# Kernel tuning notes

Measured on AMD Instinct MI355X. Metric: run time of the kernel, lower is better.

## Reference

```python
import jax, jax.numpy as jnp
import numpy as np

E = 1024   # embed_dim
H = 16     # num_heads
DH = E // H
FF = 4096  # intermediate_size
EPS = 1e-5


def layernorm(x, g, b):
    mu = jnp.mean(x, axis=-1, keepdims=True)
    var = jnp.var(x, axis=-1, keepdims=True)
    return (x - mu) * jax.lax.rsqrt(var + EPS) * g + b


def setup_inputs() -> dict:
    key = jax.random.key(0)
    ks = jax.random.split(key, 16)
    s = 0.02
    return {
        "x": jax.random.normal(ks[0], (2, 2048, E), dtype=jnp.float32),
        "ln1_g": jnp.ones((E,), jnp.float32),
        "ln1_b": jnp.zeros((E,), jnp.float32),
        "ln2_g": jnp.ones((E,), jnp.float32),
        "ln2_b": jnp.zeros((E,), jnp.float32),
        # per-head Q/K/V projections stacked: [H, E, DH]
        "wq": jax.random.normal(ks[1], (H, E, DH), jnp.float32) * s,
        "bq": jnp.zeros((H, DH), jnp.float32),
        "wk": jax.random.normal(ks[2], (H, E, DH), jnp.float32) * s,
        "bk": jnp.zeros((H, DH), jnp.float32),
        "wv": jax.random.normal(ks[3], (H, E, DH), jnp.float32) * s,
        "bv": jnp.zeros((H, DH), jnp.float32),
        "wo": jax.random.normal(ks[4], (E, E), jnp.float32) * s,
        "bo": jnp.zeros((E,), jnp.float32),
        "w1": jax.random.normal(ks[5], (E, FF), jnp.float32) * s,
        "b1": jnp.zeros((FF,), jnp.float32),
        "w2": jax.random.normal(ks[6], (FF, E), jnp.float32) * s,
        "b2": jnp.zeros((E,), jnp.float32),
    }


def reference(x, ln1_g, ln1_b, ln2_g, ln2_b, wq, bq, wk, bk, wv, bv,
              wo, bo, w1, b1, w2, b2):
    # --- multi-head attention (pre-LN) ---
    h = layernorm(x, ln1_g, ln1_b)                       # [B,S,E]
    q = jnp.einsum('bse,hed->bhsd', h, wq) + bq[:, None, :]
    k = jnp.einsum('bse,hed->bhsd', h, wk) + bk[:, None, :]
    v = jnp.einsum('bse,hed->bhsd', h, wv) + bv[:, None, :]
    scores = jnp.einsum('bhsd,bhtd->bhst', q, k) / jnp.sqrt(
        jnp.asarray(DH, x.dtype))                        # [B,H,S,S]
    w = jax.nn.softmax(scores, axis=-1)
    attn = jnp.einsum('bhst,bhtd->bhsd', w, v)           # [B,H,S,DH]
    B, _, S, _ = attn.shape
    concat = attn.transpose(0, 2, 1, 3).reshape(B, S, E)  # head concat order
    x = x + concat @ wo + bo
    # --- feed-forward (pre-LN), exact GELU, dropout_p=0 ---
    h2 = layernorm(x, ln2_g, ln2_b)
    ff = jax.nn.gelu(h2 @ w1 + b1, approximate=False) @ w2 + b2
    return x + ff
```

## Files before the change

### kernel.cpp

```cpp
#include <hip/hip_runtime.h>
#include <hip/hip_bf16.h>
#include <math.h>

typedef __attribute__((ext_vector_type(8))) short short8;
typedef __attribute__((ext_vector_type(4))) float f32x4;
typedef __attribute__((ext_vector_type(16))) float f32x16;
typedef __attribute__((ext_vector_type(4))) unsigned u32x4;

#define MFMA_BF16(a, b, c) __builtin_amdgcn_mfma_f32_16x16x32_bf16(a, b, c, 0, 0, 0)
#define MFMA32_BF16(a, b, c) __builtin_amdgcn_mfma_f32_32x32x16_bf16(a, b, c, 0, 0, 0)

#define GLD_LDS16(g, l)                                              \
  __builtin_amdgcn_global_load_lds(                                  \
      (const __attribute__((address_space(1))) void*)(g),            \
      (__attribute__((address_space(3))) void*)(l), 16, 0, 0)

__device__ __forceinline__ unsigned cvt_pk_bf16(float lo, float hi) {
  unsigned r;
  asm("v_cvt_pk_bf16_f32 %0, %1, %2" : "=v"(r) : "v"(lo), "v"(hi));
  return r;
}
#define PSWAP(a, b) asm volatile("v_permlane32_swap_b32 %0, %1" : "+v"(a), "+v"(b))

__device__ __forceinline__ unsigned short f2bf(float f) {
  union { float f; unsigned u; } v; v.f = f;
  unsigned r = v.u + 0x7FFFu + ((v.u >> 16) & 1u);
  return (unsigned short)(r >> 16);
}
__device__ __forceinline__ float bf2f(unsigned short u) {
  union { unsigned u; float f; } v; v.u = ((unsigned)u) << 16;
  return v.f;
}

__global__ __launch_bounds__(256) void transpose_cast(
    const float* __restrict__ in, unsigned short* __restrict__ out,
    int R, int C, size_t in_bs, size_t out_bs) {
  __shared__ float t[32][33];
  const float* inp = in + blockIdx.z * in_bs;
  unsigned short* outp = out + blockIdx.z * out_bs;
  const int c0 = blockIdx.x * 32, r0 = blockIdx.y * 32;
  const int tx = threadIdx.x, ty = threadIdx.y;
#pragma unroll
  for (int i = 0; i < 32; i += 8)
    t[ty + i][tx] = inp[(size_t)(r0 + ty + i) * C + c0 + tx];
  __syncthreads();
#pragma unroll
  for (int i = 0; i < 32; i += 8)
    outp[(size_t)(c0 + ty + i) * R + r0 + tx] = f2bf(t[tx][ty + i]);
}

__global__ void concat_bias(const float* __restrict__ bq, const float* __restrict__ bk,
                            const float* __restrict__ bv, float* __restrict__ bcat) {
  int i = blockIdx.x * 256 + threadIdx.x;
  if (i < 1024) bcat[i] = bq[i];
  else if (i < 2048) bcat[i] = bk[i - 1024];
  else if (i < 3072) bcat[i] = bv[i - 2048];
}

__global__ __launch_bounds__(256) void ln_kernel(
    const float* __restrict__ x, const float* __restrict__ g,
    const float* __restrict__ bb, unsigned short* __restrict__ out) {
  const int row = blockIdx.x, tid = threadIdx.x;
  const float4 v = ((const float4*)(x + (size_t)row * 1024))[tid];
  float s = v.x + v.y + v.z + v.w;
  float ss = v.x * v.x + v.y * v.y + v.z * v.z + v.w * v.w;
#pragma unroll
  for (int k = 1; k < 64; k <<= 1) {
    s += __shfl_xor(s, k, 64);
    ss += __shfl_xor(ss, k, 64);
  }
  __shared__ float red[8];
  const int wid = tid >> 6;
  if ((tid & 63) == 0) { red[wid] = s; red[wid + 4] = ss; }
  __syncthreads();
  s = red[0] + red[1] + red[2] + red[3];
  ss = red[4] + red[5] + red[6] + red[7];
  const float mu = s * (1.0f / 1024.0f);
  const float var = ss * (1.0f / 1024.0f) - mu * mu;
  const float rs = rsqrtf(var + 1e-5f);
  const float4 gv = ((const float4*)g)[tid];
  const float4 bv = ((const float4*)bb)[tid];
  ushort4 o;
  o.x = f2bf((v.x - mu) * rs * gv.x + bv.x);
  o.y = f2bf((v.y - mu) * rs * gv.y + bv.y);
  o.z = f2bf((v.z - mu) * rs * gv.z + bv.z);
  o.w = f2bf((v.w - mu) * rs * gv.w + bv.w);
  ((ushort4*)(out + (size_t)row * 1024))[tid] = o;
}

template <int EPI, int BN>
__global__ __launch_bounds__(256, 3) void gemm_bt(
    const unsigned short* __restrict__ A, const unsigned short* __restrict__ Bt,
    const float* __restrict__ bias, const float* __restrict__ res,
    void* __restrict__ Cout, int M, int N, int K) {
  constexpr int NFR = BN / 32;
  constexpr int BISS = BN / 32;
  __shared__ unsigned short As[128 * 64];
  __shared__ unsigned short Bs[BN * 64];
  const int tid = threadIdx.x;
  const int wid = tid >> 6, lane = tid & 63;
  const int li = lane & 15, gi = lane >> 4;
  const int bm = blockIdx.y, bn = blockIdx.x;
  const int wr = (wid >> 1) << 6;
  const int wc = (wid & 1) * (BN / 2);

  f32x4 acc[4][NFR];
#pragma unroll
  for (int m = 0; m < 4; ++m)
#pragma unroll
    for (int n = 0; n < NFR; ++n) acc[m][n] = (f32x4)0.0f;

  const size_t Ksz = (size_t)K;
  const int srow = tid >> 3;
  const int segG = (tid & 7) ^ (srow & 7);
  const unsigned short* Ab = A + (size_t)(bm * 128 + srow) * Ksz + segG * 8;
  const unsigned short* Bb = Bt + (size_t)(bn * BN + srow) * Ksz + segG * 8;

  for (int kt = 0; kt < K; kt += 64) {
#pragma unroll
    for (int c = 0; c < 4; ++c)
      GLD_LDS16(Ab + (size_t)(c * 32) * Ksz + kt, As + c * 2048 + wid * 512);
#pragma unroll
    for (int c = 0; c < BISS; ++c)
      GLD_LDS16(Bb + (size_t)(c * 32) * Ksz + kt, Bs + c * 2048 + wid * 512);
    __syncthreads();
    short8 af[4][2], bf[NFR][2];
#pragma unroll
    for (int m = 0; m < 4; ++m)
#pragma unroll
      for (int kk = 0; kk < 2; ++kk) {
        const int row = wr + m * 16 + li;
        af[m][kk] = *(const short8*)(As + row * 64 + ((kk * 4 + gi) ^ (row & 7)) * 8);
      }
#pragma unroll
    for (int n = 0; n < NFR; ++n)
#pragma unroll
      for (int kk = 0; kk < 2; ++kk) {
        const int row = wc + n * 16 + li;
        bf[n][kk] = *(const short8*)(Bs + row * 64 + ((kk * 4 + gi) ^ (row & 7)) * 8);
      }
    __builtin_amdgcn_s_setprio(1);
#pragma unroll
    for (int m = 0; m < 4; ++m)
#pragma unroll
      for (int n = 0; n < NFR; ++n) {
        acc[m][n] = MFMA_BF16(af[m][0], bf[n][0], acc[m][n]);
        acc[m][n] = MFMA_BF16(af[m][1], bf[n][1], acc[m][n]);
      }
    __builtin_amdgcn_s_setprio(0);
    __syncthreads();
  }

  const int row_base = bm * 128 + wr + gi * 4;
  const int col_base = bn * BN + wc + li;
#pragma unroll
  for (int m = 0; m < 4; ++m) {
#pragma unroll
    for (int n = 0; n < NFR; ++n) {
      const int col = col_base + n * 16;
      const float bi = bias[col];
#pragma unroll
      for (int r = 0; r < 4; ++r) {
        const int row = row_base + m * 16 + r;
        float v = acc[m][n][r] + bi;
        if (EPI == 2) v = 0.5f * v * (1.0f + erff(v * 0.70710678118654752f));
        const size_t idx = (size_t)row * N + col;
        if (EPI == 1) ((float*)Cout)[idx] = v + res[idx];
        else ((unsigned short*)Cout)[idx] = f2bf(v);
      }
    }
  }
}

__global__ __launch_bounds__(256, 4) void attn_kernel(
    const unsigned short* __restrict__ qkv, unsigned short* __restrict__ op0,
    unsigned short* __restrict__ op1, float* __restrict__ lpart) {
  __shared__ unsigned short Kl[2][4096];
  __shared__ unsigned VT[2][64 * 33];
  const int tid = threadIdx.x;
  const int wid = tid >> 6, lane = tid & 63;
  const int l31 = lane & 31, hiq = lane >> 5;
  const int kvh = blockIdx.z & 1, b = blockIdx.z >> 1, h = blockIdx.y;
  const int q0 = blockIdx.x * 128 + wid * 32;
  const int LD = 3072;
  const size_t base = (size_t)b * 2048 * LD;
  const size_t kvoff = (size_t)kvh * 1024 * LD;

  short8 qb[4];
  {
    const unsigned short* qp = qkv + base + (size_t)(q0 + l31) * LD + h * 64 + hiq * 8;
#pragma unroll
    for (int ds = 0; ds < 4; ++ds) qb[ds] = *(const short8*)(qp + ds * 16);
  }

  f32x16 o0 = (f32x16)0.0f, o1 = (f32x16)0.0f;
  float la = 0.0f, lb = 0.0f;

  const int krw = lane >> 3;
  const int ksegG = (lane & 7) ^ krw;
  const unsigned short* kdma = qkv + base + kvoff + 1024 + h * 64 + ksegG * 8 +
                               (size_t)(wid * 16 + krw) * LD;

  const int kp = tid >> 3, dq8 = tid & 7;
  const unsigned short* vsrc = qkv + base + kvoff + 2048 + h * 64 + dq8 * 8 +
                               (size_t)(2 * kp) * LD;

  auto kstage = [&](int buf, int t) {
    GLD_LDS16(kdma + (size_t)t * 64 * LD, &Kl[buf][wid * 1024]);
    GLD_LDS16(kdma + (size_t)(t * 64 + 8) * LD, &Kl[buf][wid * 1024 + 512]);
  };
  auto vwrite = [&](int buf, short8 a, short8 c) {
    unsigned* vd = VT[buf];
#pragma unroll
    for (int j = 0; j < 8; ++j)
      vd[(dq8 * 8 + j) * 33 + kp] =
          (unsigned)(unsigned short)a[j] | ((unsigned)(unsigned short)c[j] << 16);
  };

  kstage(0, 0);
  vwrite(0, *(const short8*)vsrc, *(const short8*)(vsrc + LD));
  __syncthreads();

  for (int t = 0; t < 16; ++t) {
    short8 va{}, vc{};
    if (t < 15) {
      kstage((t + 1) & 1, t + 1);
      const unsigned short* vs = vsrc + (size_t)(t + 1) * 64 * LD;
      va = *(const short8*)(vs);
      vc = *(const short8*)(vs + LD);
    }

    const unsigned short* kl = Kl[t & 1];
    short8 kf[2][4];
#pragma unroll
    for (int kvb = 0; kvb < 2; ++kvb)
#pragma unroll
      for (int ds = 0; ds < 4; ++ds)
        kf[kvb][ds] = *(const short8*)(
            kl + (kvb * 32 + l31) * 64 + (((2 * ds + hiq) ^ (l31 & 7)) * 8));

    f32x16 sA = (f32x16)0.0f, sB = (f32x16)0.0f;
    __builtin_amdgcn_s_setprio(1);
#pragma unroll
    for (int ds = 0; ds < 4; ++ds) {
      sA = MFMA32_BF16(kf[0][ds], qb[ds], sA);
      sB = MFMA32_BF16(kf[1][ds], qb[ds], sB);
    }
    __builtin_amdgcn_s_setprio(0);

    const unsigned short* vtb = (const unsigned short*)VT[t & 1];
#pragma unroll
    for (int kvb = 0; kvb < 2; ++kvb) {
      const f32x16 s = kvb ? sB : sA;
      unsigned P[8];
#pragma unroll
      for (int i = 0; i < 8; ++i) {
        const float pe = __expf(s[2 * i] * 0.125f);
        const float po = __expf(s[2 * i + 1] * 0.125f);
        la += pe; lb += po;
        P[i] = cvt_pk_bf16(pe, po);
      }
      PSWAP(P[0], P[2]); PSWAP(P[1], P[3]);
      PSWAP(P[4], P[6]); PSWAP(P[5], P[7]);
      const short8 pa0 = __builtin_bit_cast(short8, (u32x4){P[0], P[1], P[2], P[3]});
      const short8 pa1 = __builtin_bit_cast(short8, (u32x4){P[4], P[5], P[6], P[7]});
      const int ks0 = 2 * kvb;
      const short8 v00 = *(const short8*)(vtb + (0 * 32 + l31) * 66 + (8 * ks0 + 4 * hiq) * 2);
      const short8 v01 = *(const short8*)(vtb + (0 * 32 + l31) * 66 + (8 * ks0 + 8 + 4 * hiq) * 2);
      const short8 v10 = *(const short8*)(vtb + (1 * 32 + l31) * 66 + (8 * ks0 + 4 * hiq) * 2);
      const short8 v11 = *(const short8*)(vtb + (1 * 32 + l31) * 66 + (8 * ks0 + 8 + 4 * hiq) * 2);
      __builtin_amdgcn_s_setprio(1);
      o0 = MFMA32_BF16(pa0, v00, o0);
      o0 = MFMA32_BF16(pa1, v01, o0);
      o1 = MFMA32_BF16(pa0, v10, o1);
      o1 = MFMA32_BF16(pa1, v11, o1);
      __builtin_amdgcn_s_setprio(0);
    }

    if (t < 15) vwrite((t + 1) & 1, va, vc);
    __syncthreads();
  }

  const float lsum = la + lb;
  const float lt = lsum + __shfl_xor(lsum, 32, 64);
  if (hiq == 0)
    lpart[(size_t)kvh * 65536 + ((size_t)(b * 2048 + q0 + l31) * 16) + h] = lt;

  unsigned short* op = kvh ? op1 : op0;
#pragma unroll
  for (int r = 0; r < 16; ++r) {
    const int crow = (r & 3) + 8 * (r >> 2) + 4 * hiq;
    const size_t rowb = (size_t)(b * 2048 + q0 + crow) * 1024 + h * 64 + l31;
    op[rowb]      = f2bf(o0[r]);
    op[rowb + 32] = f2bf(o1[r]);
  }
}

__global__ __launch_bounds__(256) void attn_combine(
    const unsigned short* __restrict__ op0, unsigned short* __restrict__ op1io,
    const float* __restrict__ lpart) {
  const size_t i8 = (size_t)blockIdx.x * 256 + threadIdx.x;
  const size_t g = (i8 * 8) >> 6;
  const float inv = 1.0f / (lpart[g] + lpart[g + 65536]);
  const short8 a = *(const short8*)(op0 + i8 * 8);
  const short8 c = *(const short8*)(op1io + i8 * 8);
  short8 o;
#pragma unroll
  for (int j = 0; j < 8; ++j)
    o[j] = (short)f2bf((bf2f((unsigned short)a[j]) + bf2f((unsigned short)c[j])) * inv);
  *(short8*)(op1io + i8 * 8) = o;
}

extern "C" void kernel_launch(void* const* d_in, const int* in_sizes, int n_in,
                              void* d_out, int out_size, void* d_ws, size_t ws_size,
                              hipStream_t stream) {
  const float* x     = (const float*)d_in[0];
  const float* ln1_g = (const float*)d_in[1];
  const float* ln1_b = (const float*)d_in[2];
  const float* ln2_g = (const float*)d_in[3];
  const float* ln2_b = (const float*)d_in[4];
  const float* wq    = (const float*)d_in[5];
  const float* bq    = (const float*)d_in[6];
  const float* wk    = (const float*)d_in[7];
  const float* bk    = (const float*)d_in[8];
  const float* wv    = (const float*)d_in[9];
  const float* bv    = (const float*)d_in[10];
  const float* wo    = (const float*)d_in[11];
  const float* bo    = (const float*)d_in[12];
  const float* w1    = (const float*)d_in[13];
  const float* b1    = (const float*)d_in[14];
  const float* w2    = (const float*)d_in[15];
  const float* b2    = (const float*)d_in[16];
  float* out = (float*)d_out;

  char* p = (char*)d_ws;
  unsigned short* ws_h     = (unsigned short*)p; p += 4096ull * 1024 * 2;
  unsigned short* ws_qkv   = (unsigned short*)p; p += 4096ull * 3072 * 2;
  unsigned short* ws_attn  = (unsigned short*)p; p += 4096ull * 1024 * 2;
  unsigned short* ws_wqkvT = (unsigned short*)p; p += 3072ull * 1024 * 2;
  unsigned short* ws_woT   = (unsigned short*)p; p += 1024ull * 1024 * 2;
  unsigned short* ws_w1T   = (unsigned short*)p; p += 4096ull * 1024 * 2;
  unsigned short* ws_w2T   = (unsigned short*)p; p += 1024ull * 4096 * 2;
  float*          ws_bqkv  = (float*)p;          p += 3072 * 4;
  float*          ws_l     = (float*)p;          p += 2ull * 65536 * 4;
  unsigned short* ws_ff = ws_qkv;

  const dim3 tb(32, 8);
  transpose_cast<<<dim3(2, 32, 16), tb, 0, stream>>>(
      wq, ws_wqkvT, 1024, 64, (size_t)(1024 * 64), (size_t)(64 * 1024));
  transpose_cast<<<dim3(2, 32, 16), tb, 0, stream>>>(
      wk, ws_wqkvT + 1024ull * 1024, 1024, 64, (size_t)(1024 * 64), (size_t)(64 * 1024));
  transpose_cast<<<dim3(2, 32, 16), tb, 0, stream>>>(
      wv, ws_wqkvT + 2048ull * 1024, 1024, 64, (size_t)(1024 * 64), (size_t)(64 * 1024));
  transpose_cast<<<dim3(32, 32, 1), tb, 0, stream>>>(wo, ws_woT, 1024, 1024, 0, 0);
  transpose_cast<<<dim3(128, 32, 1), tb, 0, stream>>>(w1, ws_w1T, 1024, 4096, 0, 0);
  transpose_cast<<<dim3(32, 128, 1), tb, 0, stream>>>(w2, ws_w2T, 4096, 1024, 0, 0);
  concat_bias<<<12, 256, 0, stream>>>(bq, bk, bv, ws_bqkv);

  ln_kernel<<<4096, 256, 0, stream>>>(x, ln1_g, ln1_b, ws_h);
  gemm_bt<0, 128><<<dim3(24, 32), 256, 0, stream>>>(ws_h, ws_wqkvT, ws_bqkv, nullptr,
                                                    ws_qkv, 4096, 3072, 1024);
  attn_kernel<<<dim3(16, 16, 4), 256, 0, stream>>>(ws_qkv, ws_h, ws_attn, ws_l);
  attn_combine<<<2048, 256, 0, stream>>>(ws_h, ws_attn, ws_l);
  gemm_bt<1, 64><<<dim3(16, 32), 256, 0, stream>>>(ws_attn, ws_woT, bo, x,
                                                   out, 4096, 1024, 1024);
  ln_kernel<<<4096, 256, 0, stream>>>(out, ln2_g, ln2_b, ws_h);
  gemm_bt<2, 128><<<dim3(32, 32), 256, 0, stream>>>(ws_h, ws_w1T, b1, nullptr,
                                                    ws_ff, 4096, 4096, 1024);
  gemm_bt<1, 64><<<dim3(16, 32), 256, 0, stream>>>(ws_ff, ws_w2T, b2, out,
                                                   out, 4096, 1024, 4096);
}
```

Baseline: 284.7 us.

## Pre-transpose V into a global buffer and read V fragments directly in attention

Adds a vtrans kernel that writes V transposed per (batch, head) into a workspace aliased on the w1T buffer. The attention kernel no longer stages V through LDS with a per-tile transpose. It loads V^T fragments straight from global memory, which removes the LDS writes and the VT shared buffer. To make the aliasing safe, the w1/w2 weight transposes move after attention. The cost is an extra kernel launch and extra global traffic, and the attention kernel now issues uncoalesced, non-prefetched global loads (strided 2048 apart per lane) inside its inner loop.

Result: no change. 279.4 us (-1.9%).

```diff
diff --git a/kernel.cpp b/kernel.cpp
--- a/kernel.cpp
+++ b/kernel.cpp
@@ -55,6 +55,25 @@
   if (i < 1024) bcat[i] = bq[i];
   else if (i < 2048) bcat[i] = bk[i - 1024];
   else if (i < 3072) bcat[i] = bv[i - 2048];
+}
+
+__global__ __launch_bounds__(512) void vtrans(
+    const unsigned short* __restrict__ qkv, unsigned short* __restrict__ vt) {
+  __shared__ unsigned short t[64][65];
+  const int bh = blockIdx.y;
+  const int s0 = blockIdx.x * 64;
+  const int tx = threadIdx.x;
+  const int ty = threadIdx.y;
+  const unsigned short* in =
+      qkv + (size_t)(bh >> 4) * 2048 * 3072 + 2048 + (bh & 15) * 64;
+#pragma unroll
+  for (int i = 0; i < 8; ++i)
+    t[ty * 8 + i][tx] = in[(size_t)(s0 + ty * 8 + i) * 3072 + tx];
+  __syncthreads();
+  unsigned short* o = vt + (size_t)bh * 64 * 2048 + s0;
+#pragma unroll
+  for (int i = 0; i < 8; ++i)
+    o[(size_t)(ty * 8 + i) * 2048 + tx] = t[tx][ty * 8 + i];
 }
 
 __global__ __launch_bounds__(256) void ln_kernel(
@@ -173,10 +192,10 @@
 }
 
 __global__ __launch_bounds__(256, 4) void attn_kernel(
-    const unsigned short* __restrict__ qkv, unsigned short* __restrict__ op0,
-    unsigned short* __restrict__ op1, float* __restrict__ lpart) {
+    const unsigned short* __restrict__ qkv, const unsigned short* __restrict__ vt,
+    unsigned short* __restrict__ op0, unsigned short* __restrict__ op1,
+    float* __restrict__ lpart) {
   __shared__ unsigned short Kl[2][4096];
-  __shared__ unsigned VT[2][64 * 33];
   const int tid = threadIdx.x;
   const int wid = tid >> 6, lane = tid & 63;
   const int l31 = lane & 31, hiq = lane >> 5;
@@ -201,34 +220,19 @@
   const unsigned short* kdma = qkv + base + kvoff + 1024 + h * 64 + ksegG * 8 +
                                (size_t)(wid * 16 + krw) * LD;
 
-  const int kp = tid >> 3, dq8 = tid & 7;
-  const unsigned short* vsrc = qkv + base + kvoff + 2048 + h * 64 + dq8 * 8 +
-                               (size_t)(2 * kp) * LD;
+  const unsigned short* vbh =
+      vt + (size_t)(b * 16 + h) * 64 * 2048 + kvh * 1024 + 8 * hiq;
 
   auto kstage = [&](int buf, int t) {
     GLD_LDS16(kdma + (size_t)t * 64 * LD, &Kl[buf][wid * 1024]);
     GLD_LDS16(kdma + (size_t)(t * 64 + 8) * LD, &Kl[buf][wid * 1024 + 512]);
   };
-  auto vwrite = [&](int buf, short8 a, short8 c) {
-    unsigned* vd = VT[buf];
-#pragma unroll
-    for (int j = 0; j < 8; ++j)
-      vd[(dq8 * 8 + j) * 33 + kp] =
-          (unsigned)(unsigned short)a[j] | ((unsigned)(unsigned short)c[j] << 16);
-  };
 
   kstage(0, 0);
-  vwrite(0, *(const short8*)vsrc, *(const short8*)(vsrc + LD));
   __syncthreads();
 
   for (int t = 0; t < 16; ++t) {
-    short8 va{}, vc{};
-    if (t < 15) {
-      kstage((t + 1) & 1, t + 1);
-      const unsigned short* vs = vsrc + (size_t)(t + 1) * 64 * LD;
-      va = *(const short8*)(vs);
-      vc = *(const short8*)(vs + LD);
-    }
+    if (t < 15) kstage((t + 1) & 1, t + 1);
 
     const unsigned short* kl = Kl[t & 1];
     short8 kf[2][4];
@@ -248,9 +252,14 @@
     }
     __builtin_amdgcn_s_setprio(0);
 
-    const unsigned short* vtb = (const unsigned short*)VT[t & 1];
+    const unsigned short* vtt = vbh + 64 * t;
 #pragma unroll
     for (int kvb = 0; kvb < 2; ++kvb) {
+      const int ks0 = 2 * kvb;
+      const short8 v00 = *(const short8*)(vtt + (size_t)l31 * 2048 + 16 * ks0);
+      const short8 v01 = *(const short8*)(vtt + (size_t)l31 * 2048 + 16 * ks0 + 16);
+      const short8 v10 = *(const short8*)(vtt + (size_t)(32 + l31) * 2048 + 16 * ks0);
+      const short8 v11 = *(const short8*)(vtt + (size_t)(32 + l31) * 2048 + 16 * ks0 + 16);
       const f32x16 s = kvb ? sB : sA;
       unsigned P[8];
 #pragma unroll
@@ -264,11 +273,6 @@
       PSWAP(P[4], P[6]); PSWAP(P[5], P[7]);
       const short8 pa0 = __builtin_bit_cast(short8, (u32x4){P[0], P[1], P[2], P[3]});
       const short8 pa1 = __builtin_bit_cast(short8, (u32x4){P[4], P[5], P[6], P[7]});
-      const int ks0 = 2 * kvb;
-      const short8 v00 = *(const short8*)(vtb + (0 * 32 + l31) * 66 + (8 * ks0 + 4 * hiq) * 2);
-      const short8 v01 = *(const short8*)(vtb + (0 * 32 + l31) * 66 + (8 * ks0 + 8 + 4 * hiq) * 2);
-      const short8 v10 = *(const short8*)(vtb + (1 * 32 + l31) * 66 + (8 * ks0 + 4 * hiq) * 2);
-      const short8 v11 = *(const short8*)(vtb + (1 * 32 + l31) * 66 + (8 * ks0 + 8 + 4 * hiq) * 2);
       __builtin_amdgcn_s_setprio(1);
       o0 = MFMA32_BF16(pa0, v00, o0);
       o0 = MFMA32_BF16(pa1, v01, o0);
@@ -276,8 +280,6 @@
       o1 = MFMA32_BF16(pa1, v11, o1);
       __builtin_amdgcn_s_setprio(0);
     }
-
-    if (t < 15) vwrite((t + 1) & 1, va, vc);
     __syncthreads();
   }
 
@@ -344,6 +346,7 @@
   float*          ws_bqkv  = (float*)p;          p += 3072 * 4;
   float*          ws_l     = (float*)p;          p += 2ull * 65536 * 4;
   unsigned short* ws_ff = ws_qkv;
+  unsigned short* ws_vt = ws_w1T;
 
   const dim3 tb(32, 8);
   transpose_cast<<<dim3(2, 32, 16), tb, 0, stream>>>(
@@ -353,15 +356,16 @@
   transpose_cast<<<dim3(2, 32, 16), tb, 0, stream>>>(
       wv, ws_wqkvT + 2048ull * 1024, 1024, 64, (size_t)(1024 * 64), (size_t)(64 * 1024));
   transpose_cast<<<dim3(32, 32, 1), tb, 0, stream>>>(wo, ws_woT, 1024, 1024, 0, 0);
-  transpose_cast<<<dim3(128, 32, 1), tb, 0, stream>>>(w1, ws_w1T, 1024, 4096, 0, 0);
-  transpose_cast<<<dim3(32, 128, 1), tb, 0, stream>>>(w2, ws_w2T, 4096, 1024, 0, 0);
   concat_bias<<<12, 256, 0, stream>>>(bq, bk, bv, ws_bqkv);
 
   ln_kernel<<<4096, 256, 0, stream>>>(x, ln1_g, ln1_b, ws_h);
   gemm_bt<0, 128><<<dim3(24, 32), 256, 0, stream>>>(ws_h, ws_wqkvT, ws_bqkv, nullptr,
                                                     ws_qkv, 4096, 3072, 1024);
-  attn_kernel<<<dim3(16, 16, 4), 256, 0, stream>>>(ws_qkv, ws_h, ws_attn, ws_l);
+  vtrans<<<dim3(32, 32), dim3(64, 8), 0, stream>>>(ws_qkv, ws_vt);
+  attn_kernel<<<dim3(16, 16, 4), 256, 0, stream>>>(ws_qkv, ws_vt, ws_h, ws_attn, ws_l);
   attn_combine<<<2048, 256, 0, stream>>>(ws_h, ws_attn, ws_l);
+  transpose_cast<<<dim3(128, 32, 1), tb, 0, stream>>>(w1, ws_w1T, 1024, 4096, 0, 0);
+  transpose_cast<<<dim3(32, 128, 1), tb, 0, stream>>>(w2, ws_w2T, 4096, 1024, 0, 0);
   gemm_bt<1, 64><<<dim3(16, 32), 256, 0, stream>>>(ws_attn, ws_woT, bo, x,
                                                    out, 4096, 1024, 1024);
   ln_kernel<<<4096, 256, 0, stream>>>(out, ln2_g, ln2_b, ws_h);
```
